# Optimization experiments

Measured on AMD Instinct MI355X. Metric: run time of the kernel, lower is better.

Reference implementation:

```python
import jax, jax.numpy as jnp
import numpy as np

B, CIN, COUT = 16, 32, 64
H = W = 64
K = 3                      # kernel side
GRID_SIZE, SPLINE_ORDER = 5, 3
P = K * K                  # in_features of each KANLinear
GR0, GR1 = -1.0, 1.0       # grid_range


def make_grid():
    # torch: grid = arange(-k, G+k+1)*h + grid_range[0], expanded to (in_features, G+2k+1)
    h = (GR1 - GR0) / GRID_SIZE
    g = jnp.arange(-SPLINE_ORDER, GRID_SIZE + SPLINE_ORDER + 1, dtype=jnp.float32) * h + GR0
    return jnp.broadcast_to(g, (P, g.shape[0]))


def b_splines(x, grid):
    # Cox-de Boor recursion. x: (..., P) -> bases: (..., P, GRID_SIZE+SPLINE_ORDER)
    xe = x[..., None]
    bases = ((xe >= grid[:, :-1]) & (xe < grid[:, 1:])).astype(x.dtype)
    for j in range(1, SPLINE_ORDER + 1):
        left = (xe - grid[:, : -(j + 1)]) / (grid[:, j:-1] - grid[:, : -(j + 1)])
        right = (grid[:, j + 1 :] - xe) / (grid[:, j + 1 :] - grid[:, 1:-j])
        bases = left * bases[..., :-1] + right * bases[..., 1:]
    return bases


def setup_inputs() -> dict:
    key = jax.random.key(0)
    k1, k2, k3, k4 = jax.random.split(key, 4)
    x = jax.random.normal(k1, (B, CIN, H, W), dtype=jnp.float32)
    base_weight = jax.random.normal(k2, (COUT, CIN, P), dtype=jnp.float32) * (1.0 / np.sqrt(P))
    spline_weight = jax.random.normal(k3, (COUT, CIN, P, GRID_SIZE + SPLINE_ORDER), dtype=jnp.float32) * 0.1
    spline_scaler = jax.random.normal(k4, (COUT, CIN, P), dtype=jnp.float32) * (1.0 / np.sqrt(P))
    return {"x": x, "base_weight": base_weight, "spline_weight": spline_weight, "spline_scaler": spline_scaler}


def reference(x, base_weight, spline_weight, spline_scaler):
    grid = make_grid()
    # im2col like torch.nn.Unfold: (B, CIN*P, Hout, Wout), channel-major feature order
    patches = jax.lax.conv_general_dilated_patches(x, (K, K), (1, 1), "VALID")
    _, _, Ho, Wo = patches.shape
    patches = patches.reshape(B, CIN, P, Ho * Wo).transpose(0, 1, 3, 2)  # (B, CIN, L, P)
    # base branch: SiLU(x) @ base_weight^T, summed over input channels per output channel
    base_out = jnp.einsum("bclp,ocp->bol", jax.nn.silu(patches), base_weight)
    # spline branch: B-spline bases contracted with scaled spline weights
    bases = b_splines(patches, grid)                       # (B, CIN, L, P, G+k)
    scaled_w = spline_weight * spline_scaler[..., None]    # (COUT, CIN, P, G+k)
    spline_out = jnp.einsum("bclpg,ocpg->bol", bases, scaled_w)
    return (base_out + spline_out).reshape(B, COUT, Ho, Wo)
```

## Files before the change

kernel.cpp:

```cpp
#include <hip/hip_runtime.h>


typedef short v8s __attribute__((ext_vector_type(8)));
typedef float v4f __attribute__((ext_vector_type(4)));
typedef int   v4i __attribute__((ext_vector_type(4)));
typedef int   v8i __attribute__((ext_vector_type(8)));

#define FSPL8_OFF   0u
#define FSILU_OFF   16777472u
#define WMX_OFF     20972032u
#define WF8_OFF     21103104u
#define WPACKS_OFF  21119488u

#define SCALE1 0x7F7F7F7Fu

__device__ __forceinline__ unsigned short f2bf(float f) {
  unsigned int u = __float_as_uint(f);
  u += 0x7fffu + ((u >> 16) & 1u);
  return (unsigned short)(u >> 16);
}

__global__ __launch_bounds__(256) void k_feat(const float* __restrict__ x,
                                              unsigned char* __restrict__ ws) {
  const int bid = blockIdx.x;
  const int b = bid >> 6, y = bid & 63;
  const int t = threadIdx.x;
  const int xx = t & 63, cg = t >> 6;
  unsigned short h[8];
#pragma unroll
  for (int k = 0; k < 8; ++k) {
    const int c = cg * 8 + k;
    const float v = x[(((size_t)(b * 32 + c) * 64 + y) * 64) + xx];
    h[k] = f2bf(v / (1.0f + __expf(-v)));
    float bb[11];
#pragma unroll
    for (int i = 0; i < 11; ++i) {
      float t0 = -2.2f + 0.4f * i;
      bb[i] = (v >= t0 && v < t0 + 0.4f) ? 1.0f : 0.0f;
    }
#pragma unroll
    for (int j = 1; j <= 3; ++j) {
      float rj = 1.0f / (0.4f * j);
#pragma unroll
      for (int i = 0; i + j < 11; ++i) {
        float ti = -2.2f + 0.4f * i;
        bb[i] = (v - ti) * rj * bb[i] + ((ti + 0.4f * (j + 1)) - v) * rj * bb[i + 1];
      }
    }
    uint2 o;
    unsigned w0 = __builtin_amdgcn_cvt_pk_fp8_f32(bb[0], bb[1], 0, false);
    w0 = __builtin_amdgcn_cvt_pk_fp8_f32(bb[2], bb[3], w0, true);
    unsigned w1 = __builtin_amdgcn_cvt_pk_fp8_f32(bb[4], bb[5], 0, false);
    w1 = __builtin_amdgcn_cvt_pk_fp8_f32(bb[6], bb[7], w1, true);
    o.x = w0; o.y = w1;
    *(uint2*)(ws + FSPL8_OFF + ((((size_t)(b * 32 + c) * 64 + y) * 64) + xx) * 8) = o;
  }
  uint4 s;
  s.x = (unsigned)h[0] | ((unsigned)h[1] << 16);
  s.y = (unsigned)h[2] | ((unsigned)h[3] << 16);
  s.z = (unsigned)h[4] | ((unsigned)h[5] << 16);
  s.w = (unsigned)h[6] | ((unsigned)h[7] << 16);
  *(uint4*)(ws + FSILU_OFF + (size_t)(b * 4096 + y * 64 + xx) * 64 + cg * 16) = s;
}

__global__ __launch_bounds__(256) void k_wpack(const float* __restrict__ bw,
                                               const float* __restrict__ sw,
                                               const float* __restrict__ sc,
                                               unsigned char* __restrict__ ws) {
  int tid = blockIdx.x * 256 + threadIdx.x;
  if (tid >= 165888) return;
  if (tid < 147456) {
    int k, dst;
    if (tid < 131072) {
      int bh = tid & 15, lane = (tid >> 4) & 63, pc = (tid >> 10) & 1;
      int ss = (tid >> 13) & 1, p = tid >> 14;
      k = p * 288 + ss * 128 + (lane >> 4) * 32 + pc * 16 + bh;
      dst = WMX_OFF + tid;
    } else {
      int t2 = tid - 131072;
      int e = t2 & 7, lane = (t2 >> 3) & 63, p = t2 >> 11;
      k = p * 288 + 256 + (lane >> 4) * 8 + e;
      dst = WF8_OFF + t2;
    }
    int ot = (tid < 131072) ? ((tid >> 11) & 3) : (((tid - 131072) >> 9) & 3);
    int lane = (tid < 131072) ? ((tid >> 4) & 63) : (((tid - 131072) >> 3) & 63);
    int o = (ot << 4) + (lane & 15);
    int chunk = k / 24, u = k - chunk * 24;
    int dj = u >> 3, g = u & 7;
    int c = chunk / 3, di = chunk - c * 3;
    int p_tap = di * 3 + dj;
    float val = sw[((size_t)(o * 32 + c) * 9 + p_tap) * 8 + g] *
                sc[(size_t)(o * 32 + c) * 9 + p_tap];
    ws[dst] = (unsigned char)(__builtin_amdgcn_cvt_pk_fp8_f32(val, 0.f, 0, false) & 0xff);
  } else {
    int t2 = tid - 147456;
    int e = t2 & 7, lane = (t2 >> 3) & 63, ot = (t2 >> 9) & 3, sp = t2 >> 11;
    int o = (ot << 4) + (lane & 15);
    int cc = ((lane >> 4) << 3) + e;
    float val = bw[(size_t)(o * 32 + cc) * 9 + sp];
    *(unsigned short*)(ws + WPACKS_OFF + (size_t)t2 * 2) = f2bf(val);
  }
}

__device__ __forceinline__ void ld16(unsigned char* ldsp, const unsigned char* gp) {
  __builtin_amdgcn_global_load_lds(
      (const __attribute__((address_space(1))) unsigned int*)gp,
      (__attribute__((address_space(3))) unsigned int*)ldsp, 16, 0, 0);
}

__global__ __launch_bounds__(512) void k_gemm(const unsigned char* __restrict__ ws,
                                              float* __restrict__ out) {
  __shared__ __align__(16) unsigned char wl8[2][18432];
  __shared__ __align__(16) unsigned char fl8[2][12544];
  __shared__ __align__(16) unsigned char wsil[36864];
  __shared__ __align__(16) unsigned char fsil[25088];

  const int blk = blockIdx.x;
  const int b = blk >> 4, ig = blk & 15;
  const int i0 = ig * 4;
  const int tid = threadIdx.x;
  const int wave = tid >> 6, lane = tid & 63;
  const int q = lane >> 4, ln = lane & 15;
  const int r = wave >> 1, oh = wave & 1;
  const int i = i0 + r;

  auto stage_spl = [&](int p, int bi) {
#pragma unroll
    for (int it = 0; it < 4; ++it) {
      const int u = wave + it * 8;
      if (u < 16) {
        ld16(&wl8[bi][u * 1024], ws + WMX_OFF + (size_t)p * 16384 + (size_t)u * 1024 + lane * 16);
      } else if (u < 18) {
        ld16(&wl8[bi][u * 1024], ws + WF8_OFF + (size_t)p * 2048 + (size_t)(u - 16) * 1024 + lane * 16);
      } else if (u < 30) {
        const int v = u - 18;
        const int cp = v / 3, cr = v - cp * 3;
        ld16(&fl8[bi][v * 1024],
             ws + FSPL8_OFF + ((size_t)((b * 32 + p * 4 + cp) * 64 + i0 + cr * 2)) * 512 + lane * 16);
      }
    }
  };

  auto stage_silu = [&]() {
#pragma unroll
    for (int it = 0; it < 8; ++it) {
      const int u = wave + it * 8;
      if (u < 36) {
        ld16(&wsil[u * 1024], ws + WPACKS_OFF + (size_t)u * 1024 + lane * 16);
      } else if (u < 60) {
        const int v = u - 36;
        const int rr = v >> 2, p4 = v & 3;
        const int y = min(i0 + rr, 63);
        ld16(&fsil[v * 1024],
             ws + FSILU_OFF + (size_t)(b * 64 + y) * 4096 +
                 (p4 * 16 + (lane >> 2)) * 64 + ((lane & 3) ^ ((lane >> 2) & 3)) * 16);
      }
    }
  };

  auto offf = [&](int sg, int qq) {
    int rid = 4 * sg + qq;
    int ch = rid / 3, sub = rid - ch * 3;
    int cp = ch / 3, di = ch - cp * 3;
    return cp * 3072 + (r + di) * 512 + (sub + ln) * 8;
  };
  int offA[4], offB[4];
#pragma unroll
  for (int qq = 0; qq < 4; ++qq) { offA[qq] = offf(q, qq); offB[qq] = offf(4 + q, qq); }
  const int off8 = offf(8, q);

  v4f acc[2][4];
#pragma unroll
  for (int a = 0; a < 2; ++a)
#pragma unroll
    for (int c = 0; c < 4; ++c) acc[a][c] = (v4f){0.f, 0.f, 0.f, 0.f};

  stage_silu();
  stage_spl(0, 0);
  __syncthreads();

#pragma unroll 1
  for (int t = 0; t < 8; ++t) {
    if (t < 7) stage_spl(t + 1, (t + 1) & 1);
    const unsigned char* wb = wl8[t & 1];
    const unsigned char* fb = fl8[t & 1];
#pragma unroll
    for (int ss = 0; ss < 2; ++ss) {
      union { v8i v; v4i h[2]; } wf[2];
#pragma unroll
      for (int tt = 0; tt < 2; ++tt) {
        const unsigned char* wp = wb + ss * 8192 + (oh * 2 + tt) * 2048 + lane * 16;
        wf[tt].h[0] = *(const v4i*)(wp);
        wf[tt].h[1] = *(const v4i*)(wp + 1024);
      }
      const int* offs = ss ? offB : offA;
      union { v8i v; long l[4]; } ff[4];
#pragma unroll
      for (int pt = 0; pt < 4; ++pt)
#pragma unroll
        for (int qq = 0; qq < 4; ++qq)
          ff[pt].l[qq] = *(const long*)(fb + offs[qq] + pt * 128);
#pragma unroll
      for (int tt = 0; tt < 2; ++tt)
#pragma unroll
        for (int pt = 0; pt < 4; ++pt)
          acc[tt][pt] = __builtin_amdgcn_mfma_scale_f32_16x16x128_f8f6f4(
              wf[tt].v, ff[pt].v, acc[tt][pt], 0, 0, 0, SCALE1, 0, SCALE1);
    }
    {
      long w8[2], f8[4];
#pragma unroll
      for (int tt = 0; tt < 2; ++tt)
        w8[tt] = *(const long*)(wb + 16384 + (oh * 2 + tt) * 512 + lane * 8);
#pragma unroll
      for (int pt = 0; pt < 4; ++pt)
        f8[pt] = *(const long*)(fb + off8 + pt * 128);
#pragma unroll
      for (int tt = 0; tt < 2; ++tt)
#pragma unroll
        for (int pt = 0; pt < 4; ++pt)
          acc[tt][pt] = __builtin_amdgcn_mfma_f32_16x16x32_fp8_fp8(
              w8[tt], f8[pt], acc[tt][pt], 0, 0, 0);
    }
    __syncthreads();
  }

#pragma unroll
  for (int e = 0; e < 9; ++e) {
    const int di = e / 3, dj = e % 3;
    v8s wb2[2], fb2[4];
#pragma unroll
    for (int tt = 0; tt < 2; ++tt)
      wb2[tt] = *(const v8s*)(&wsil[0] + e * 4096 + (oh * 2 + tt) * 1024 + lane * 16);
    const int xb = dj + ln;
    const int sbase = (r + di) * 4096 + xb * 64 + ((q ^ (xb & 3)) * 16);
#pragma unroll
    for (int pt = 0; pt < 4; ++pt)
      fb2[pt] = *(const v8s*)(&fsil[0] + sbase + pt * 1024);
#pragma unroll
    for (int tt = 0; tt < 2; ++tt)
#pragma unroll
      for (int pt = 0; pt < 4; ++pt)
        acc[tt][pt] = __builtin_amdgcn_mfma_f32_16x16x32_bf16(
            wb2[tt], fb2[pt], acc[tt][pt], 0, 0, 0);
  }

  if (i < 62) {
#pragma unroll
    for (int tt = 0; tt < 2; ++tt)
#pragma unroll
      for (int pt = 0; pt < 4; ++pt) {
        const int j = pt * 16 + ln;
        if (j < 62) {
#pragma unroll
          for (int rr = 0; rr < 4; ++rr) {
            const int o = (oh * 2 + tt) * 16 + q * 4 + rr;
            out[(((size_t)b * 64 + o) * 62 + i) * 62 + j] = acc[tt][pt][rr];
          }
        }
      }
  }
}

extern "C" void kernel_launch(void* const* d_in, const int* in_sizes, int n_in,
                              void* d_out, int out_size, void* d_ws, size_t ws_size,
                              hipStream_t stream) {
  const float* x  = (const float*)d_in[0];
  const float* bw = (const float*)d_in[1];
  const float* sw = (const float*)d_in[2];
  const float* sc = (const float*)d_in[3];
  unsigned char* ws = (unsigned char*)d_ws;
  float* out = (float*)d_out;

  hipLaunchKernelGGL(k_feat,  dim3(1024), dim3(256), 0, stream, x, ws);
  hipLaunchKernelGGL(k_wpack, dim3(648),  dim3(256), 0, stream, bw, sw, sc, ws);
  hipLaunchKernelGGL(k_gemm,  dim3(256),  dim3(512), 0, stream, ws, out);
}
```

Baseline: 102.3 us.

## Merge feature and weight prep kernels; compute only four nonzero B-spline bases

Folds the weight-packing kernel into the feature kernel as extra blocks, so one launch is removed and the two independent prep jobs can run concurrently. It also replaces the full 11-element Cox-de Boor recursion with a closed-form evaluation of the four nonzero cubic bases for the knot interval, then shifts the packed fp8 bytes into position. This cuts per-element ALU work in the feature pass. The risk is small numerical differences at knot boundaries, plus the shift and clamp logic for edge intervals.

```diff
diff --git a/kernel.cpp b/kernel.cpp
--- a/kernel.cpp
+++ b/kernel.cpp
@@ -20,9 +20,48 @@
   return (unsigned short)(u >> 16);
 }
 
-__global__ __launch_bounds__(256) void k_feat(const float* __restrict__ x,
+__global__ __launch_bounds__(256) void k_prep(const float* __restrict__ x,
+                                              const float* __restrict__ bw,
+                                              const float* __restrict__ sw,
+                                              const float* __restrict__ sc,
                                               unsigned char* __restrict__ ws) {
   const int bid = blockIdx.x;
+  if (bid >= 1024) {
+    int tid = (bid - 1024) * 256 + threadIdx.x;
+    if (tid >= 165888) return;
+    if (tid < 147456) {
+      int k, dst;
+      if (tid < 131072) {
+        int bh = tid & 15, lane = (tid >> 4) & 63, pc = (tid >> 10) & 1;
+        int ss = (tid >> 13) & 1, p = tid >> 14;
+        k = p * 288 + ss * 128 + (lane >> 4) * 32 + pc * 16 + bh;
+        dst = WMX_OFF + tid;
+      } else {
+        int t2 = tid - 131072;
+        int e = t2 & 7, lane = (t2 >> 3) & 63, p = t2 >> 11;
+        k = p * 288 + 256 + (lane >> 4) * 8 + e;
+        dst = WF8_OFF + t2;
+      }
+      int ot = (tid < 131072) ? ((tid >> 11) & 3) : (((tid - 131072) >> 9) & 3);
+      int lane = (tid < 131072) ? ((tid >> 4) & 63) : (((tid - 131072) >> 3) & 63);
+      int o = (ot << 4) + (lane & 15);
+      int chunk = k / 24, u = k - chunk * 24;
+      int dj = u >> 3, g = u & 7;
+      int c = chunk / 3, di = chunk - c * 3;
+      int p_tap = di * 3 + dj;
+      float val = sw[((size_t)(o * 32 + c) * 9 + p_tap) * 8 + g] *
+                  sc[(size_t)(o * 32 + c) * 9 + p_tap];
+      ws[dst] = (unsigned char)(__builtin_amdgcn_cvt_pk_fp8_f32(val, 0.f, 0, false) & 0xff);
+    } else {
+      int t2 = tid - 147456;
+      int e = t2 & 7, lane = (t2 >> 3) & 63, ot = (t2 >> 9) & 3, sp = t2 >> 11;
+      int o = (ot << 4) + (lane & 15);
+      int cc = ((lane >> 4) << 3) + e;
+      float val = bw[(size_t)(o * 32 + cc) * 9 + sp];
+      *(unsigned short*)(ws + WPACKS_OFF + (size_t)t2 * 2) = f2bf(val);
+    }
+    return;
+  }
   const int b = bid >> 6, y = bid & 63;
   const int t = threadIdx.x;
   const int xx = t & 63, cg = t >> 6;
@@ -32,74 +71,38 @@
     const int c = cg * 8 + k;
     const float v = x[(((size_t)(b * 32 + c) * 64 + y) * 64) + xx];
     h[k] = f2bf(v / (1.0f + __expf(-v)));
-    float bb[11];
-#pragma unroll
-    for (int i = 0; i < 11; ++i) {
-      float t0 = -2.2f + 0.4f * i;
-      bb[i] = (v >= t0 && v < t0 + 0.4f) ? 1.0f : 0.0f;
-    }
-#pragma unroll
-    for (int j = 1; j <= 3; ++j) {
-      float rj = 1.0f / (0.4f * j);
-#pragma unroll
-      for (int i = 0; i + j < 11; ++i) {
-        float ti = -2.2f + 0.4f * i;
-        bb[i] = (v - ti) * rj * bb[i] + ((ti + 0.4f * (j + 1)) - v) * rj * bb[i + 1];
-      }
-    }
+    float s = (v + 2.2f) * 2.5f;
+    int i0 = (int)floorf(s);
+    i0 = i0 < 0 ? 0 : (i0 > 10 ? 10 : i0);
+    const float u = (v + 2.2f) - 0.4f * (float)i0;
+    float N0 = (0.4f - u) * 2.5f;
+    float N1 = u * 2.5f;
+    float a0 = N0 * 1.25f, a1 = N1 * 1.25f;
+    N0 = (0.4f - u) * a0;
+    float N2 = u * a1;
+    N1 = (u + 0.4f) * a0 + (0.8f - u) * a1;
+    float b0 = N0 * (1.0f / 1.2f), b1 = N1 * (1.0f / 1.2f), b2 = N2 * (1.0f / 1.2f);
+    N0 = (0.4f - u) * b0;
+    float N3 = u * b2;
+    N1 = (u + 0.8f) * b0 + (0.8f - u) * b1;
+    N2 = (u + 0.4f) * b1 + (1.2f - u) * b2;
+    unsigned w0 = __builtin_amdgcn_cvt_pk_fp8_f32(N0, N1, 0, false);
+    w0 = __builtin_amdgcn_cvt_pk_fp8_f32(N2, N3, w0, true);
+    unsigned long long wd = w0;
+    const int sh = i0 * 8 - 24;
+    wd = (sh >= 0) ? (wd << sh) : (wd >> (-sh));
+    if (!(v >= -2.2f && v < 2.2f)) wd = 0;
     uint2 o;
-    unsigned w0 = __builtin_amdgcn_cvt_pk_fp8_f32(bb[0], bb[1], 0, false);
-    w0 = __builtin_amdgcn_cvt_pk_fp8_f32(bb[2], bb[3], w0, true);
-    unsigned w1 = __builtin_amdgcn_cvt_pk_fp8_f32(bb[4], bb[5], 0, false);
-    w1 = __builtin_amdgcn_cvt_pk_fp8_f32(bb[6], bb[7], w1, true);
-    o.x = w0; o.y = w1;
+    o.x = (unsigned)wd;
+    o.y = (unsigned)(wd >> 32);
     *(uint2*)(ws + FSPL8_OFF + ((((size_t)(b * 32 + c) * 64 + y) * 64) + xx) * 8) = o;
   }
-  uint4 s;
-  s.x = (unsigned)h[0] | ((unsigned)h[1] << 16);
-  s.y = (unsigned)h[2] | ((unsigned)h[3] << 16);
-  s.z = (unsigned)h[4] | ((unsigned)h[5] << 16);
-  s.w = (unsigned)h[6] | ((unsigned)h[7] << 16);
-  *(uint4*)(ws + FSILU_OFF + (size_t)(b * 4096 + y * 64 + xx) * 64 + cg * 16) = s;
-}
-
-__global__ __launch_bounds__(256) void k_wpack(const float* __restrict__ bw,
-                                               const float* __restrict__ sw,
-                                               const float* __restrict__ sc,
-                                               unsigned char* __restrict__ ws) {
-  int tid = blockIdx.x * 256 + threadIdx.x;
-  if (tid >= 165888) return;
-  if (tid < 147456) {
-    int k, dst;
-    if (tid < 131072) {
-      int bh = tid & 15, lane = (tid >> 4) & 63, pc = (tid >> 10) & 1;
-      int ss = (tid >> 13) & 1, p = tid >> 14;
-      k = p * 288 + ss * 128 + (lane >> 4) * 32 + pc * 16 + bh;
-      dst = WMX_OFF + tid;
-    } else {
-      int t2 = tid - 131072;
-      int e = t2 & 7, lane = (t2 >> 3) & 63, p = t2 >> 11;
-      k = p * 288 + 256 + (lane >> 4) * 8 + e;
-      dst = WF8_OFF + t2;
-    }
-    int ot = (tid < 131072) ? ((tid >> 11) & 3) : (((tid - 131072) >> 9) & 3);
-    int lane = (tid < 131072) ? ((tid >> 4) & 63) : (((tid - 131072) >> 3) & 63);
-    int o = (ot << 4) + (lane & 15);
-    int chunk = k / 24, u = k - chunk * 24;
-    int dj = u >> 3, g = u & 7;
-    int c = chunk / 3, di = chunk - c * 3;
-    int p_tap = di * 3 + dj;
-    float val = sw[((size_t)(o * 32 + c) * 9 + p_tap) * 8 + g] *
-                sc[(size_t)(o * 32 + c) * 9 + p_tap];
-    ws[dst] = (unsigned char)(__builtin_amdgcn_cvt_pk_fp8_f32(val, 0.f, 0, false) & 0xff);
-  } else {
-    int t2 = tid - 147456;
-    int e = t2 & 7, lane = (t2 >> 3) & 63, ot = (t2 >> 9) & 3, sp = t2 >> 11;
-    int o = (ot << 4) + (lane & 15);
-    int cc = ((lane >> 4) << 3) + e;
-    float val = bw[(size_t)(o * 32 + cc) * 9 + sp];
-    *(unsigned short*)(ws + WPACKS_OFF + (size_t)t2 * 2) = f2bf(val);
-  }
+  uint4 sv;
+  sv.x = (unsigned)h[0] | ((unsigned)h[1] << 16);
+  sv.y = (unsigned)h[2] | ((unsigned)h[3] << 16);
+  sv.z = (unsigned)h[4] | ((unsigned)h[5] << 16);
+  sv.w = (unsigned)h[6] | ((unsigned)h[7] << 16);
+  *(uint4*)(ws + FSILU_OFF + (size_t)(b * 4096 + y * 64 + xx) * 64 + cg * 16) = sv;
 }
 
 __device__ __forceinline__ void ld16(unsigned char* ldsp, const unsigned char* gp) {
@@ -272,7 +275,6 @@
   unsigned char* ws = (unsigned char*)d_ws;
   float* out = (float*)d_out;
 
-  hipLaunchKernelGGL(k_feat,  dim3(1024), dim3(256), 0, stream, x, ws);
-  hipLaunchKernelGGL(k_wpack, dim3(648),  dim3(256), 0, stream, bw, sw, sc, ws);
-  hipLaunchKernelGGL(k_gemm,  dim3(256),  dim3(512), 0, stream, ws, out);
-}
+  hipLaunchKernelGGL(k_prep, dim3(1672), dim3(256), 0, stream, x, bw, sw, sc, ws);
+  hipLaunchKernelGGL(k_gemm, dim3(256),  dim3(512), 0, stream, ws, out);
+}
```

New measurement: 93.69 us. 1.09x faster.

## Fuse feature computation into GEMM kernel with closed-form cubic B-spline

Applied to the files above, without the earlier changes.

Removes the separate feature kernel, which wrote fp8 spline bases and bf16 SiLU values to workspace. The GEMM kernel now reads x directly, computes SiLU and the four nonzero cubic B-spline bases in closed form, and writes them into LDS. The global loads for the next channel group are issued before the MFMAs of the current step, and the LDS stores happen after them. This cuts a kernel launch and a large workspace round trip, at the cost of recomputing features for overlapping rows in each block and extra ALU work inside the GEMM loop.

```diff
diff --git a/kernel.cpp b/kernel.cpp
--- a/kernel.cpp
+++ b/kernel.cpp
@@ -6,8 +6,6 @@
 typedef int   v4i __attribute__((ext_vector_type(4)));
 typedef int   v8i __attribute__((ext_vector_type(8)));
 
-#define FSPL8_OFF   0u
-#define FSILU_OFF   16777472u
 #define WMX_OFF     20972032u
 #define WF8_OFF     21103104u
 #define WPACKS_OFF  21119488u
@@ -18,49 +16,6 @@
   unsigned int u = __float_as_uint(f);
   u += 0x7fffu + ((u >> 16) & 1u);
   return (unsigned short)(u >> 16);
-}
-
-__global__ __launch_bounds__(256) void k_feat(const float* __restrict__ x,
-                                              unsigned char* __restrict__ ws) {
-  const int bid = blockIdx.x;
-  const int b = bid >> 6, y = bid & 63;
-  const int t = threadIdx.x;
-  const int xx = t & 63, cg = t >> 6;
-  unsigned short h[8];
-#pragma unroll
-  for (int k = 0; k < 8; ++k) {
-    const int c = cg * 8 + k;
-    const float v = x[(((size_t)(b * 32 + c) * 64 + y) * 64) + xx];
-    h[k] = f2bf(v / (1.0f + __expf(-v)));
-    float bb[11];
-#pragma unroll
-    for (int i = 0; i < 11; ++i) {
-      float t0 = -2.2f + 0.4f * i;
-      bb[i] = (v >= t0 && v < t0 + 0.4f) ? 1.0f : 0.0f;
-    }
-#pragma unroll
-    for (int j = 1; j <= 3; ++j) {
-      float rj = 1.0f / (0.4f * j);
-#pragma unroll
-      for (int i = 0; i + j < 11; ++i) {
-        float ti = -2.2f + 0.4f * i;
-        bb[i] = (v - ti) * rj * bb[i] + ((ti + 0.4f * (j + 1)) - v) * rj * bb[i + 1];
-      }
-    }
-    uint2 o;
-    unsigned w0 = __builtin_amdgcn_cvt_pk_fp8_f32(bb[0], bb[1], 0, false);
-    w0 = __builtin_amdgcn_cvt_pk_fp8_f32(bb[2], bb[3], w0, true);
-    unsigned w1 = __builtin_amdgcn_cvt_pk_fp8_f32(bb[4], bb[5], 0, false);
-    w1 = __builtin_amdgcn_cvt_pk_fp8_f32(bb[6], bb[7], w1, true);
-    o.x = w0; o.y = w1;
-    *(uint2*)(ws + FSPL8_OFF + ((((size_t)(b * 32 + c) * 64 + y) * 64) + xx) * 8) = o;
-  }
-  uint4 s;
-  s.x = (unsigned)h[0] | ((unsigned)h[1] << 16);
-  s.y = (unsigned)h[2] | ((unsigned)h[3] << 16);
-  s.z = (unsigned)h[4] | ((unsigned)h[5] << 16);
-  s.w = (unsigned)h[6] | ((unsigned)h[7] << 16);
-  *(uint4*)(ws + FSILU_OFF + (size_t)(b * 4096 + y * 64 + xx) * 64 + cg * 16) = s;
 }
 
 __global__ __launch_bounds__(256) void k_wpack(const float* __restrict__ bw,
@@ -109,6 +64,7 @@
 }
 
 __global__ __launch_bounds__(512) void k_gemm(const unsigned char* __restrict__ ws,
+                                              const float* __restrict__ x,
                                               float* __restrict__ out) {
   __shared__ __align__(16) unsigned char wl8[2][18432];
   __shared__ __align__(16) unsigned char fl8[2][12544];
@@ -124,37 +80,76 @@
   const int r = wave >> 1, oh = wave & 1;
   const int i = i0 + r;
 
-  auto stage_spl = [&](int p, int bi) {
-#pragma unroll
-    for (int it = 0; it < 4; ++it) {
+  const bool factive = tid < 384;
+  const int frow = tid >> 6, fx = tid & 63;
+  const int fy = min(i0 + frow, 63);
+
+  auto stage_w = [&](int p, int bi) {
+#pragma unroll
+    for (int it = 0; it < 3; ++it) {
       const int u = wave + it * 8;
       if (u < 16) {
         ld16(&wl8[bi][u * 1024], ws + WMX_OFF + (size_t)p * 16384 + (size_t)u * 1024 + lane * 16);
       } else if (u < 18) {
         ld16(&wl8[bi][u * 1024], ws + WF8_OFF + (size_t)p * 2048 + (size_t)(u - 16) * 1024 + lane * 16);
-      } else if (u < 30) {
-        const int v = u - 18;
-        const int cp = v / 3, cr = v - cp * 3;
-        ld16(&fl8[bi][v * 1024],
-             ws + FSPL8_OFF + ((size_t)((b * 32 + p * 4 + cp) * 64 + i0 + cr * 2)) * 512 + lane * 16);
-      }
-    }
-  };
-
-  auto stage_silu = [&]() {
-#pragma unroll
-    for (int it = 0; it < 8; ++it) {
+      }
+    }
+  };
+
+  auto stage_wsil = [&]() {
+#pragma unroll
+    for (int it = 0; it < 5; ++it) {
       const int u = wave + it * 8;
-      if (u < 36) {
-        ld16(&wsil[u * 1024], ws + WPACKS_OFF + (size_t)u * 1024 + lane * 16);
-      } else if (u < 60) {
-        const int v = u - 36;
-        const int rr = v >> 2, p4 = v & 3;
-        const int y = min(i0 + rr, 63);
-        ld16(&fsil[v * 1024],
-             ws + FSILU_OFF + (size_t)(b * 64 + y) * 4096 +
-                 (p4 * 16 + (lane >> 2)) * 64 + ((lane & 3) ^ ((lane >> 2) & 3)) * 16);
-      }
+      if (u < 36) ld16(&wsil[u * 1024], ws + WPACKS_OFF + (size_t)u * 1024 + lane * 16);
+    }
+  };
+
+  auto feat_load = [&](int p, float* v) {
+    if (factive) {
+#pragma unroll
+      for (int cp = 0; cp < 4; ++cp)
+        v[cp] = x[((size_t)(b * 32 + p * 4 + cp) * 64 + fy) * 64 + fx];
+    }
+  };
+
+  auto feat_store = [&](int p, int bi, const float* v) {
+    if (factive) {
+      unsigned long long spl[4];
+      unsigned short hh[4];
+#pragma unroll
+      for (int cp = 0; cp < 4; ++cp) {
+        const float vv = v[cp];
+        hh[cp] = f2bf(vv / (1.0f + __expf(-vv)));
+        float s = (vv + 2.2f) * 2.5f;
+        int ii = (int)floorf(s);
+        ii = ii < 0 ? 0 : (ii > 10 ? 10 : ii);
+        const float uu = (vv + 2.2f) - 0.4f * (float)ii;
+        float N0 = (0.4f - uu) * 2.5f;
+        float N1 = uu * 2.5f;
+        float a0 = N0 * 1.25f, a1 = N1 * 1.25f;
+        N0 = (0.4f - uu) * a0;
+        float N2 = uu * a1;
+        N1 = (uu + 0.4f) * a0 + (0.8f - uu) * a1;
+        float c0 = N0 * (1.0f / 1.2f), c1 = N1 * (1.0f / 1.2f), c2 = N2 * (1.0f / 1.2f);
+        N0 = (0.4f - uu) * c0;
+        float N3 = uu * c2;
+        N1 = (uu + 0.8f) * c0 + (0.8f - uu) * c1;
+        N2 = (uu + 0.4f) * c1 + (1.2f - uu) * c2;
+        unsigned w0 = __builtin_amdgcn_cvt_pk_fp8_f32(N0, N1, 0, false);
+        w0 = __builtin_amdgcn_cvt_pk_fp8_f32(N2, N3, w0, true);
+        unsigned long long wd = w0;
+        const int sh = ii * 8 - 24;
+        wd = (sh >= 0) ? (wd << sh) : (wd >> (-sh));
+        if (!(vv >= -2.2f && vv < 2.2f)) wd = 0;
+        spl[cp] = wd;
+      }
+#pragma unroll
+      for (int cp = 0; cp < 4; ++cp)
+        *(unsigned long long*)(&fl8[bi][cp * 3072 + frow * 512 + fx * 8]) = spl[cp];
+      unsigned long long sp = (unsigned long long)((unsigned)hh[0] | ((unsigned)hh[1] << 16)) |
+                              ((unsigned long long)((unsigned)hh[2] | ((unsigned)hh[3] << 16)) << 32);
+      *(unsigned long long*)(&fsil[frow * 4096 + fx * 64 +
+                                   (((p >> 1) ^ (fx & 3)) * 16) + (p & 1) * 8]) = sp;
     }
   };
 
@@ -175,13 +170,22 @@
 #pragma unroll
     for (int c = 0; c < 4; ++c) acc[a][c] = (v4f){0.f, 0.f, 0.f, 0.f};
 
-  stage_silu();
-  stage_spl(0, 0);
+  stage_wsil();
+  stage_w(0, 0);
+  {
+    float v0[4];
+    feat_load(0, v0);
+    feat_store(0, 0, v0);
+  }
   __syncthreads();
 
 #pragma unroll 1
   for (int t = 0; t < 8; ++t) {
-    if (t < 7) stage_spl(t + 1, (t + 1) & 1);
+    float vbuf[4];
+    if (t < 7) {
+      stage_w(t + 1, (t + 1) & 1);
+      feat_load(t + 1, vbuf);
+    }
     const unsigned char* wb = wl8[t & 1];
     const unsigned char* fb = fl8[t & 1];
 #pragma unroll
@@ -222,6 +226,7 @@
           acc[tt][pt] = __builtin_amdgcn_mfma_f32_16x16x32_fp8_fp8(
               w8[tt], f8[pt], acc[tt][pt], 0, 0, 0);
     }
+    if (t < 7) feat_store(t + 1, (t + 1) & 1, vbuf);
     __syncthreads();
   }
 
@@ -272,7 +277,6 @@
   unsigned char* ws = (unsigned char*)d_ws;
   float* out = (float*)d_out;
 
-  hipLaunchKernelGGL(k_feat,  dim3(1024), dim3(256), 0, stream, x, ws);
-  hipLaunchKernelGGL(k_wpack, dim3(648),  dim3(256), 0, stream, bw, sw, sc, ws);
-  hipLaunchKernelGGL(k_gemm,  dim3(256),  dim3(512), 0, stream, ws, out);
-}
+  hipLaunchKernelGGL(k_wpack, dim3(648), dim3(256), 0, stream, bw, sw, sc, ws);
+  hipLaunchKernelGGL(k_gemm,  dim3(256), dim3(512), 0, stream, ws, x, out);
+}
```

Measured after the change: 92.05 us. 1.11x faster.
